# Kernel optimization log

Hardware: AMD Instinct MI355X
Metric: run time of the kernel (lower is better)

Reference implementation:

```python
import jax, jax.numpy as jnp
import numpy as np

B, N, T, C = 16, 12, 128, 128  # batch, num_classes (nodes), temporal, channels


def _bn(x, gamma, beta, eps=1e-5):
    # BatchNorm2d in training mode: stats over (batch, t, c), channel axis 1, biased var
    mean = jnp.mean(x, axis=(0, 2, 3), keepdims=True)
    var = jnp.var(x, axis=(0, 2, 3), keepdims=True)
    xn = (x - mean) * jax.lax.rsqrt(var + eps)
    return xn * gamma[None, :, None, None] + beta[None, :, None, None]


def setup_inputs() -> dict:
    key = jax.random.key(0)
    ks = jax.random.split(key, 3)
    scale = np.float32(np.sqrt(2.0 / C))
    inp = {
        'x': jax.random.normal(ks[0], (B, N, T, C), dtype=jnp.float32),
        'edge': jax.random.normal(ks[1], (B, N * N, T, C), dtype=jnp.float32),
    }
    wk = jax.random.split(ks[2], 10)
    for name, k in zip(['A1', 'B1', 'E1', 'U1', 'V1', 'A2', 'B2', 'E2', 'U2', 'V2'], wk):
        inp[name] = jax.random.normal(k, (C, C), dtype=jnp.float32) * scale
    for name, dim in [('g_e1', N * N), ('b_e1', N * N), ('g_v1', N), ('b_v1', N),
                      ('g_e2', N * N), ('b_e2', N * N), ('g_v2', N), ('b_v2', N)]:
        inp[name] = jnp.ones((dim,), jnp.float32) if name[0] == 'g' else jnp.zeros((dim,), jnp.float32)
    return inp


def _forward(x, edge, A1, B1, E1, U1, V1, A2, B2, E2, U2, V2,
             g_e1, b_e1, g_v1, b_v1, g_e2, b_e2, g_v2, b_v2):
    # create_e_matrix: edge index e = i*N + j; 'end' selects node i, 'start' selects node j.
    # Dense incidence einsums become pure gathers; the transpose einsum is a
    # scatter-add over j, i.e. a reshape + sum.
    i_idx = jnp.repeat(jnp.arange(N), N)  # end-node of each edge
    j_idx = jnp.tile(jnp.arange(N), N)    # start-node of each edge
    b, _, t, c = x.shape

    def layer(x, edge, A, Bw, E, U, V, ge, be, gv, bv, mask_node):
        res = x
        edge_upd = (x @ A.T)[:, i_idx] + (x @ Bw.T)[:, j_idx] + edge @ E.T
        edge_upd = _bn(edge_upd, ge, be)
        edge_upd = jnp.where(jnp.isnan(edge_upd), 0.0, edge_upd)
        edge = edge + jax.nn.relu(edge_upd)
        e = jax.nn.sigmoid(edge)
        e = jax.nn.softmax(e.reshape(b, N, N, t, c), axis=2).reshape(b, N * N, t, c)
        Ujx = (x @ V.T)[:, j_idx]
        agg = (e * Ujx).reshape(b, N, N, t, c).sum(axis=2) / N  # scatter to end nodes
        xn = _bn(x @ U.T + agg, gv, bv)
        if mask_node:  # original only NaN-masks node BN in layer 1
            xn = jnp.where(jnp.isnan(xn), 0.0, xn)
        return jax.nn.relu(res + xn), edge

    x, edge = layer(x, edge, A1, B1, E1, U1, V1, g_e1, b_e1, g_v1, b_v1, True)
    x, edge = layer(x, edge, A2, B2, E2, U2, V2, g_e2, b_e2, g_v2, b_v2, False)
    return x, edge


def reference(x, edge, A1, B1, E1, U1, V1, A2, B2, E2, U2, V2,
              g_e1, b_e1, g_v1, b_v1, g_e2, b_e2, g_v2, b_v2):
    return _forward(x, edge, A1, B1, E1, U1, V1, A2, B2, E2, U2, V2,
                    g_e1, b_e1, g_v1, b_v1, g_e2, b_e2, g_v2, b_v2)
```

## Files before the change

### kernel.cpp

```cpp
#include <hip/hip_runtime.h>
#include <hip/hip_bf16.h>

#define BB 16
#define NN 12
#define NE 144
#define TT 128
#define CC 128

typedef __attribute__((ext_vector_type(8))) short v8s;
typedef __attribute__((ext_vector_type(4))) short v4s;
typedef __attribute__((ext_vector_type(4))) float v4f;

__device__ __forceinline__ short f2bf(float f) {
    unsigned u = __float_as_uint(f);
    u += 0x7fffu + ((u >> 16) & 1u);
    return (short)(u >> 16);
}
__device__ __forceinline__ float bf2f(unsigned short u) {
    return __uint_as_float(((unsigned)u) << 16);
}
__device__ __forceinline__ v4s f4_to_bf4(float4 a) {
    v4s r; r[0] = f2bf(a.x); r[1] = f2bf(a.y); r[2] = f2bf(a.z); r[3] = f2bf(a.w); return r;
}
__device__ __forceinline__ float4 bf4_to_f4(v4s a) {
    float4 r;
    r.x = bf2f((unsigned short)a[0]); r.y = bf2f((unsigned short)a[1]);
    r.z = bf2f((unsigned short)a[2]); r.w = bf2f((unsigned short)a[3]);
    return r;
}
__device__ __forceinline__ size_t eslot(int b, int e, int t) {
    return ((((size_t)b * NE + e) * TT + t) * CC) * 2;
}

__global__ __launch_bounds__(256) void kW(
    const float* A1, const float* B1, const float* E1, const float* U1, const float* V1,
    const float* A2, const float* B2, const float* E2, const float* U2, const float* V2,
    unsigned short* wb)
{
    int idx = blockIdx.x * 256 + threadIdx.x;
    int w = idx >> 14, r = idx & 16383;
    const float* s;
    switch (w) {
        case 0: s = A1; break; case 1: s = B1; break; case 2: s = E1; break;
        case 3: s = U1; break; case 4: s = V1; break; case 5: s = A2; break;
        case 6: s = B2; break; case 7: s = E2; break; case 8: s = U2; break;
        default: s = V2; break;
    }
    wb[idx] = (unsigned short)f2bf(s[r]);
}

__global__ __launch_bounds__(256) void kP(
    const float* __restrict__ x, const unsigned short* __restrict__ wb,
    int sA, int sB, int sV, int sU,
    unsigned short* __restrict__ oA, unsigned short* __restrict__ oB,
    unsigned short* __restrict__ oV, unsigned short* __restrict__ oU)
{
    __shared__ unsigned short xt[64][136];
    int tid = threadIdx.x;
    int m0 = blockIdx.x * 64;
    #pragma unroll
    for (int it = 0; it < 8; ++it) {
        int f = it * 256 + tid;
        int row = f >> 5, c4 = f & 31;
        float4 v = *reinterpret_cast<const float4*>(x + (size_t)m0 * 128 + (size_t)f * 4);
        *reinterpret_cast<v4s*>(&xt[row][c4 * 4]) = f4_to_bf4(v);
    }
    __syncthreads();
    int lane = tid & 63, wid = tid >> 6;
    int l15 = lane & 15, l4 = lane >> 4;

    const unsigned short* Ws[4] = { wb + (size_t)sA * 16384, wb + (size_t)sB * 16384,
                                    wb + (size_t)sV * 16384, wb + (size_t)sU * 16384 };
    unsigned short* Os[4] = { oA, oB, oV, oU };

    #pragma unroll
    for (int w = 0; w < 4; ++w) {
        const unsigned short* W = Ws[w];
        unsigned short* out = Os[w];
        v8s bfr[2][4];
        #pragma unroll
        for (int nt2 = 0; nt2 < 2; ++nt2) {
            int col = (wid * 2 + nt2) * 16 + l15;
            #pragma unroll
            for (int kk = 0; kk < 4; ++kk)
                bfr[nt2][kk] = *reinterpret_cast<const v8s*>(W + col * 128 + kk * 32 + l4 * 8);
        }
        v4f acc[4][2] = {};
        #pragma unroll
        for (int kk = 0; kk < 4; ++kk) {
            #pragma unroll
            for (int mt = 0; mt < 4; ++mt) {
                v8s a = *reinterpret_cast<const v8s*>(&xt[mt * 16 + l15][kk * 32 + l4 * 8]);
                acc[mt][0] = __builtin_amdgcn_mfma_f32_16x16x32_bf16(a, bfr[0][kk], acc[mt][0], 0, 0, 0);
                acc[mt][1] = __builtin_amdgcn_mfma_f32_16x16x32_bf16(a, bfr[1][kk], acc[mt][1], 0, 0, 0);
            }
        }
        #pragma unroll
        for (int mt = 0; mt < 4; ++mt) {
            #pragma unroll
            for (int nt2 = 0; nt2 < 2; ++nt2) {
                int col = (wid * 2 + nt2) * 16 + l15;
                #pragma unroll
                for (int reg = 0; reg < 4; ++reg) {
                    int rowg = m0 + mt * 16 + l4 * 4 + reg;
                    out[(size_t)rowg * 128 + col] = (unsigned short)f2bf(acc[mt][nt2][reg]);
                }
            }
        }
    }
}

template<bool IN_F32>
__global__ __launch_bounds__(256) void kA(
    const float* __restrict__ ef32, const unsigned short* ebf,
    unsigned short* ebout,
    const unsigned short* __restrict__ xA, const unsigned short* __restrict__ xB,
    const unsigned short* __restrict__ Ebf, float* __restrict__ epart)
{
    __shared__ unsigned short ebt[48][136];
    __shared__ float4 xab4[16][33];
    __shared__ float srow[48], qrow[48];
    int tid = threadIdx.x;
    int bid = blockIdx.x;
    int third = bid % 3; int bt = bid / 3;
    int b = bt >> 7, t = bt & 127;
    if (tid < 48) { srow[tid] = 0.f; qrow[tid] = 0.f; }

    if constexpr (IN_F32) {
        const float* eb = ef32 + (((size_t)(b * NE + third * 48) * TT) + t) * CC;
        #pragma unroll
        for (int it = 0; it < 6; ++it) {
            int f = it * 256 + tid;
            int row = f >> 5, c4 = f & 31;
            float4 v = *reinterpret_cast<const float4*>(eb + (size_t)row * (TT * CC) + c4 * 4);
            *reinterpret_cast<v4s*>(&ebt[row][c4 * 4]) = f4_to_bf4(v);
        }
    } else {
        #pragma unroll
        for (int it = 0; it < 3; ++it) {
            int f = it * 256 + tid;
            int row = f >> 4, c8 = f & 15;
            *reinterpret_cast<v8s*>(&ebt[row][c8 * 8]) =
                *reinterpret_cast<const v8s*>(ebf + eslot(b, third * 48 + row, t) + c8 * 8);
        }
    }
    #pragma unroll
    for (int it = 0; it < 2; ++it) {
        int f = it * 256 + tid;
        int row = f >> 5, c4 = f & 31;
        const unsigned short* src = (row < 4)
            ? (xA + (((size_t)(b * NN + third * 4 + row) * TT) + t) * CC)
            : (xB + (((size_t)(b * NN + (row - 4)) * TT) + t) * CC);
        v4s v = *reinterpret_cast<const v4s*>(src + c4 * 4);
        xab4[row][c4] = bf4_to_f4(v);
    }
    __syncthreads();
    if constexpr (IN_F32) {
        #pragma unroll
        for (int it = 0; it < 3; ++it) {
            int f = it * 256 + tid;
            int row = f >> 4, c8 = f & 15;
            *reinterpret_cast<v8s*>(ebout + eslot(b, third * 48 + row, t) + c8 * 8) =
                *reinterpret_cast<const v8s*>(&ebt[row][c8 * 8]);
        }
    }
    int lane = tid & 63, wid = tid >> 6;
    int l15 = lane & 15, l4 = lane >> 4;
    v8s bfr[2][4];
    #pragma unroll
    for (int nt2 = 0; nt2 < 2; ++nt2) {
        int col = (wid * 2 + nt2) * 16 + l15;
        #pragma unroll
        for (int kk = 0; kk < 4; ++kk)
            bfr[nt2][kk] = *reinterpret_cast<const v8s*>(Ebf + col * 128 + kk * 32 + l4 * 8);
    }
    v4f acc[3][2] = {};
    #pragma unroll
    for (int kk = 0; kk < 4; ++kk) {
        #pragma unroll
        for (int mt = 0; mt < 3; ++mt) {
            v8s a = *reinterpret_cast<const v8s*>(&ebt[mt * 16 + l15][kk * 32 + l4 * 8]);
            acc[mt][0] = __builtin_amdgcn_mfma_f32_16x16x32_bf16(a, bfr[0][kk], acc[mt][0], 0, 0, 0);
            acc[mt][1] = __builtin_amdgcn_mfma_f32_16x16x32_bf16(a, bfr[1][kk], acc[mt][1], 0, 0, 0);
        }
    }
    const float* xabf = reinterpret_cast<const float*>(xab4);
    #pragma unroll
    for (int mt = 0; mt < 3; ++mt) {
        #pragma unroll
        for (int reg = 0; reg < 4; ++reg) {
            int r = mt * 16 + l4 * 4 + reg;
            int il = r / 12, jl = r - il * 12;
            float s = 0.f, q = 0.f;
            #pragma unroll
            for (int nt2 = 0; nt2 < 2; ++nt2) {
                int col = (wid * 2 + nt2) * 16 + l15;
                float v = acc[mt][nt2][reg] + xabf[il * 132 + col] + xabf[(4 + jl) * 132 + col];
                s += v; q += v * v;
            }
            #pragma unroll
            for (int off = 1; off < 16; off <<= 1) { s += __shfl_xor(s, off); q += __shfl_xor(q, off); }
            if (l15 == 0) { atomicAdd(&srow[r], s); atomicAdd(&qrow[r], q); }
        }
    }
    __syncthreads();
    if (tid < 48) {
        epart[(size_t)bid * 96 + tid * 2 + 0] = srow[tid];
        epart[(size_t)bid * 96 + tid * 2 + 1] = qrow[tid];
    }
}

__global__ __launch_bounds__(256) void kRede(
    const float* __restrict__ epart, const float* __restrict__ g,
    const float* __restrict__ be, float* __restrict__ estats)
{
    int e = blockIdx.x;
    int third = e / 48, le = e % 48;
    float s = 0.f, q = 0.f;
    for (int bt = threadIdx.x; bt < 2048; bt += 256) {
        const float* p = epart + ((size_t)(bt * 3 + third) * 96 + le * 2);
        s += p[0]; q += p[1];
    }
    __shared__ float ss[4], qq[4];
    #pragma unroll
    for (int off = 32; off >= 1; off >>= 1) { s += __shfl_down(s, off); q += __shfl_down(q, off); }
    int wid = threadIdx.x >> 6;
    if ((threadIdx.x & 63) == 0) { ss[wid] = s; qq[wid] = q; }
    __syncthreads();
    if (threadIdx.x == 0) {
        s = ss[0] + ss[1] + ss[2] + ss[3];
        q = qq[0] + qq[1] + qq[2] + qq[3];
        const float M = 262144.f;
        float mean = s / M;
        float var = q / M - mean * mean;
        float sc = g[e] * rsqrtf(var + 1e-5f);
        estats[e * 2] = sc;
        estats[e * 2 + 1] = be[e] - mean * sc;
    }
}

template<bool OUT_F32>
__global__ __launch_bounds__(256) void kC(
    const unsigned short* ebuf,
    unsigned short* ebout_bf,
    float* edge_out_f32,
    const unsigned short* __restrict__ xA, const unsigned short* __restrict__ xB,
    const unsigned short* __restrict__ xV, const unsigned short* __restrict__ xU,
    const unsigned short* __restrict__ Ebf, const float* __restrict__ estats,
    unsigned short* __restrict__ yout, float* __restrict__ npart)
{
    __shared__ unsigned short ebt[48][136];
    __shared__ float4 xab4[28][33];
    __shared__ float scs[48], shs[48];
    __shared__ float ns[4], nq[4];
    int tid = threadIdx.x;
    int bid = blockIdx.x;
    int third = bid % 3; int bt = bid / 3;
    int b = bt >> 7, t = bt & 127;
    if (tid < 48) { scs[tid] = estats[(third * 48 + tid) * 2]; shs[tid] = estats[(third * 48 + tid) * 2 + 1]; }
    if (tid < 4) { ns[tid] = 0.f; nq[tid] = 0.f; }
    #pragma unroll
    for (int it = 0; it < 3; ++it) {
        int f = it * 256 + tid;
        int row = f >> 4, c8 = f & 15;
        *reinterpret_cast<v8s*>(&ebt[row][c8 * 8]) =
            *reinterpret_cast<const v8s*>(ebuf + eslot(b, third * 48 + row, t) + c8 * 8);
    }
    #pragma unroll
    for (int it = 0; it < 4; ++it) {
        int f = it * 256 + tid;
        if (f < 896) {
            int row = f >> 5, c4 = f & 31;
            const unsigned short* src;
            if (row < 4)       src = xA + (((size_t)(b * NN + third * 4 + row) * TT) + t) * CC;
            else if (row < 16) src = xB + (((size_t)(b * NN + (row - 4)) * TT) + t) * CC;
            else               src = xV + (((size_t)(b * NN + (row - 16)) * TT) + t) * CC;
            v4s v = *reinterpret_cast<const v4s*>(src + c4 * 4);
            xab4[row][c4] = bf4_to_f4(v);
        }
    }
    __syncthreads();
    int lane = tid & 63, wid = tid >> 6;
    int l15 = lane & 15, l4 = lane >> 4;
    v8s bfr[2][4];
    #pragma unroll
    for (int nt2 = 0; nt2 < 2; ++nt2) {
        int col = (wid * 2 + nt2) * 16 + l15;
        #pragma unroll
        for (int kk = 0; kk < 4; ++kk)
            bfr[nt2][kk] = *reinterpret_cast<const v8s*>(Ebf + col * 128 + kk * 32 + l4 * 8);
    }
    v4f acc[3][2] = {};
    #pragma unroll
    for (int kk = 0; kk < 4; ++kk) {
        #pragma unroll
        for (int mt = 0; mt < 3; ++mt) {
            v8s a = *reinterpret_cast<const v8s*>(&ebt[mt * 16 + l15][kk * 32 + l4 * 8]);
            acc[mt][0] = __builtin_amdgcn_mfma_f32_16x16x32_bf16(a, bfr[0][kk], acc[mt][0], 0, 0, 0);
            acc[mt][1] = __builtin_amdgcn_mfma_f32_16x16x32_bf16(a, bfr[1][kk], acc[mt][1], 0, 0, 0);
        }
    }
    __syncthreads();
    const float* xabf = reinterpret_cast<const float*>(xab4);
    #pragma unroll
    for (int mt = 0; mt < 3; ++mt) {
        #pragma unroll
        for (int reg = 0; reg < 4; ++reg) {
            int r = mt * 16 + l4 * 4 + reg;
            int il = r / 12, jl = r - il * 12;
            int eg = third * 48 + r;
            float scv = scs[r], shv = shs[r];
            #pragma unroll
            for (int nt2 = 0; nt2 < 2; ++nt2) {
                int col = (wid * 2 + nt2) * 16 + l15;
                float v = acc[mt][nt2][reg] + xabf[il * 132 + col] + xabf[(4 + jl) * 132 + col];
                float bn = scv * v + shv;
                float en = bf2f(ebt[r][col]) + fmaxf(bn, 0.f);
                ebt[r][col] = (unsigned short)f2bf(en);
                if constexpr (OUT_F32)
                    edge_out_f32[((size_t)(b * NE + eg) * TT + t) * CC + col] = en;
            }
        }
    }
    __syncthreads();
    if constexpr (!OUT_F32) {
        #pragma unroll
        for (int it = 0; it < 3; ++it) {
            int f = it * 256 + tid;
            int row = f >> 4, c8 = f & 15;
            *reinterpret_cast<v8s*>(ebout_bf + eslot(b, third * 48 + row, t) + c8 * 8) =
                *reinterpret_cast<const v8s*>(&ebt[row][c8 * 8]);
        }
    }
    #pragma unroll
    for (int ph = 0; ph < 2; ++ph) {
        int unit = tid + ph * 256;
        int il = unit >> 7, c = unit & 127;
        float den = 0.f, ag = 0.f;
        #pragma unroll
        for (int j = 0; j < 12; ++j) {
            float sv = bf2f(ebt[il * 12 + j][c]);
            float sg = 1.f / (1.f + __expf(-sv));
            float ev = __expf(sg);
            den += ev;
            ag += ev * xabf[(16 + j) * 132 + c];
        }
        float agg = ag / (den * 12.f);
        int i = third * 4 + il;
        size_t xa = (((size_t)(b * NN + i) * TT) + t) * CC + c;
        float yv = bf2f(xU[xa]) + agg;
        unsigned short us = (unsigned short)f2bf(yv);
        yout[xa] = us;
        float yr = bf2f(us);
        float s1 = yr, s2 = yr * yr;
        #pragma unroll
        for (int off = 1; off < 64; off <<= 1) { s1 += __shfl_xor(s1, off); s2 += __shfl_xor(s2, off); }
        if (lane == 0) { atomicAdd(&ns[il], s1); atomicAdd(&nq[il], s2); }
    }
    __syncthreads();
    if (tid < 4) {
        npart[(size_t)bid * 8 + tid * 2 + 0] = ns[tid];
        npart[(size_t)bid * 8 + tid * 2 + 1] = nq[tid];
    }
}

__global__ __launch_bounds__(256) void kRedn(
    const float* __restrict__ npart, const float* __restrict__ g,
    const float* __restrict__ be, float* __restrict__ nstats)
{
    int n = blockIdx.x;
    int third = n >> 2, il = n & 3;
    float s = 0.f, q = 0.f;
    for (int bt = threadIdx.x; bt < 2048; bt += 256) {
        const float* p = npart + ((size_t)(bt * 3 + third) * 8 + il * 2);
        s += p[0]; q += p[1];
    }
    __shared__ float ss[4], qq[4];
    #pragma unroll
    for (int off = 32; off >= 1; off >>= 1) { s += __shfl_down(s, off); q += __shfl_down(q, off); }
    int wid = threadIdx.x >> 6;
    if ((threadIdx.x & 63) == 0) { ss[wid] = s; qq[wid] = q; }
    __syncthreads();
    if (threadIdx.x == 0) {
        s = ss[0] + ss[1] + ss[2] + ss[3];
        q = qq[0] + qq[1] + qq[2] + qq[3];
        const float M = 262144.f;
        float mean = s / M;
        float var = q / M - mean * mean;
        float sc = g[n] * rsqrtf(var + 1e-5f);
        nstats[n * 2] = sc;
        nstats[n * 2 + 1] = be[n] - mean * sc;
    }
}

__global__ __launch_bounds__(256) void kE(
    const float* xres, const unsigned short* __restrict__ yin,
    const float* __restrict__ nstats, float* xout)
{
    int idx4 = blockIdx.x * 256 + threadIdx.x;
    size_t base = (size_t)idx4 * 4;
    int n = (int)((base >> 14) % 12);
    float scv = nstats[n * 2], shv = nstats[n * 2 + 1];
    float4 xv = *reinterpret_cast<const float4*>(xres + base);
    float4 yv = bf4_to_f4(*reinterpret_cast<const v4s*>(yin + base));
    float4 o;
    o.x = fmaxf(xv.x + scv * yv.x + shv, 0.f);
    o.y = fmaxf(xv.y + scv * yv.y + shv, 0.f);
    o.z = fmaxf(xv.z + scv * yv.z + shv, 0.f);
    o.w = fmaxf(xv.w + scv * yv.w + shv, 0.f);
    *reinterpret_cast<float4*>(xout + base) = o;
}

extern "C" void kernel_launch(void* const* d_in, const int* in_sizes, int n_in,
                              void* d_out, int out_size, void* d_ws, size_t ws_size,
                              hipStream_t stream)
{
    const float* x0 = (const float*)d_in[0];
    const float* e0 = (const float*)d_in[1];
    const float* W[10];
    for (int i = 0; i < 10; ++i) W[i] = (const float*)d_in[2 + i];
    const float* ge1 = (const float*)d_in[12];
    const float* be1 = (const float*)d_in[13];
    const float* gv1 = (const float*)d_in[14];
    const float* bv1 = (const float*)d_in[15];
    const float* ge2 = (const float*)d_in[16];
    const float* be2 = (const float*)d_in[17];
    const float* gv2 = (const float*)d_in[18];
    const float* bv2 = (const float*)d_in[19];

    const size_t SZX = (size_t)BB * NN * TT * CC;
    float* out_x = (float*)d_out;
    float* out_e = out_x + SZX;
    unsigned short* ebuf = (unsigned short*)out_e;

    unsigned short* ws16 = (unsigned short*)d_ws;
    unsigned short* xA = ws16;
    unsigned short* xB = ws16 + SZX;
    unsigned short* xV = ws16 + 2 * SZX;
    unsigned short* xU = ws16 + 3 * SZX;
    unsigned short* yb = ws16 + 4 * SZX;
    float* fpart  = (float*)(ws16 + 5 * SZX);
    float* epart  = fpart;
    float* estats = epart + 589824;
    float* npart  = estats + 288;
    float* nstats = npart + 49152;
    unsigned short* wb = (unsigned short*)(nstats + 24);

    float* x1 = out_x;

    kW<<<640, 256, 0, stream>>>(W[0], W[1], W[2], W[3], W[4], W[5], W[6], W[7], W[8], W[9], wb);

    kP<<<384, 256, 0, stream>>>(x0, wb, 0, 1, 4, 3, xA, xB, xV, xU);
    kA<true><<<6144, 256, 0, stream>>>(e0, nullptr, ebuf, xA, xB, wb + 2 * 16384, epart);
    kRede<<<144, 256, 0, stream>>>(epart, ge1, be1, estats);
    kC<false><<<6144, 256, 0, stream>>>(ebuf, ebuf, nullptr, xA, xB, xV, xU,
                                        wb + 2 * 16384, estats, yb, npart);
    kRedn<<<12, 256, 0, stream>>>(npart, gv1, bv1, nstats);
    kE<<<3072, 256, 0, stream>>>(x0, yb, nstats, x1);

    kP<<<384, 256, 0, stream>>>(x1, wb, 5, 6, 9, 8, xA, xB, xV, xU);
    kA<false><<<6144, 256, 0, stream>>>(nullptr, ebuf, nullptr, xA, xB, wb + 7 * 16384, epart);
    kRede<<<144, 256, 0, stream>>>(epart, ge2, be2, estats);
    kC<true><<<6144, 256, 0, stream>>>(ebuf, nullptr, out_e, xA, xB, xV, xU,
                                       wb + 7 * 16384, estats, yb, npart);
    kRedn<<<12, 256, 0, stream>>>(npart, gv2, bv2, nstats);
    kE<<<3072, 256, 0, stream>>>(x1, yb, nstats, out_x);
}
```

Measured before the change: 310.1 us.

## Store pre-BN edge update in kA instead of recomputing GEMM in kC

```diff
diff --git a/kernel.cpp b/kernel.cpp
--- a/kernel.cpp
+++ b/kernel.cpp
@@ -22,14 +22,8 @@
 __device__ __forceinline__ v4s f4_to_bf4(float4 a) {
     v4s r; r[0] = f2bf(a.x); r[1] = f2bf(a.y); r[2] = f2bf(a.z); r[3] = f2bf(a.w); return r;
 }
-__device__ __forceinline__ float4 bf4_to_f4(v4s a) {
-    float4 r;
-    r.x = bf2f((unsigned short)a[0]); r.y = bf2f((unsigned short)a[1]);
-    r.z = bf2f((unsigned short)a[2]); r.w = bf2f((unsigned short)a[3]);
-    return r;
-}
-__device__ __forceinline__ size_t eslot(int b, int e, int t) {
-    return ((((size_t)b * NE + e) * TT + t) * CC) * 2;
+__device__ __forceinline__ size_t ebfslot(int b, int e, int t) {
+    return (((size_t)(b * NE + e) * TT) + t) * CC;
 }
 
 __global__ __launch_bounds__(256) void kW(
@@ -112,13 +106,14 @@
 
 template<bool IN_F32>
 __global__ __launch_bounds__(256) void kA(
-    const float* __restrict__ ef32, const unsigned short* ebf,
-    unsigned short* ebout,
+    const float* __restrict__ ef32, const unsigned short* __restrict__ ebf_in,
+    unsigned short* __restrict__ ebf_out,
+    unsigned short* __restrict__ updg,
     const unsigned short* __restrict__ xA, const unsigned short* __restrict__ xB,
     const unsigned short* __restrict__ Ebf, float* __restrict__ epart)
 {
     __shared__ unsigned short ebt[48][136];
-    __shared__ float4 xab4[16][33];
+    __shared__ unsigned short xab[16][136];
     __shared__ float srow[48], qrow[48];
     int tid = threadIdx.x;
     int bid = blockIdx.x;
@@ -127,7 +122,7 @@
     if (tid < 48) { srow[tid] = 0.f; qrow[tid] = 0.f; }
 
     if constexpr (IN_F32) {
-        const float* eb = ef32 + (((size_t)(b * NE + third * 48) * TT) + t) * CC;
+        const float* eb = ef32 + ebfslot(b, third * 48, t);
         #pragma unroll
         for (int it = 0; it < 6; ++it) {
             int f = it * 256 + tid;
@@ -141,18 +136,15 @@
             int f = it * 256 + tid;
             int row = f >> 4, c8 = f & 15;
             *reinterpret_cast<v8s*>(&ebt[row][c8 * 8]) =
-                *reinterpret_cast<const v8s*>(ebf + eslot(b, third * 48 + row, t) + c8 * 8);
-        }
-    }
-    #pragma unroll
-    for (int it = 0; it < 2; ++it) {
-        int f = it * 256 + tid;
-        int row = f >> 5, c4 = f & 31;
+                *reinterpret_cast<const v8s*>(ebf_in + ebfslot(b, third * 48 + row, t) + c8 * 8);
+        }
+    }
+    {
+        int row = tid >> 4, c8 = tid & 15;
         const unsigned short* src = (row < 4)
             ? (xA + (((size_t)(b * NN + third * 4 + row) * TT) + t) * CC)
             : (xB + (((size_t)(b * NN + (row - 4)) * TT) + t) * CC);
-        v4s v = *reinterpret_cast<const v4s*>(src + c4 * 4);
-        xab4[row][c4] = bf4_to_f4(v);
+        *reinterpret_cast<v8s*>(&xab[row][c8 * 8]) = *reinterpret_cast<const v8s*>(src + c8 * 8);
     }
     __syncthreads();
     if constexpr (IN_F32) {
@@ -160,7 +152,7 @@
         for (int it = 0; it < 3; ++it) {
             int f = it * 256 + tid;
             int row = f >> 4, c8 = f & 15;
-            *reinterpret_cast<v8s*>(ebout + eslot(b, third * 48 + row, t) + c8 * 8) =
+            *reinterpret_cast<v8s*>(ebf_out + ebfslot(b, third * 48 + row, t) + c8 * 8) =
                 *reinterpret_cast<const v8s*>(&ebt[row][c8 * 8]);
         }
     }
@@ -184,7 +176,7 @@
             acc[mt][1] = __builtin_amdgcn_mfma_f32_16x16x32_bf16(a, bfr[1][kk], acc[mt][1], 0, 0, 0);
         }
     }
-    const float* xabf = reinterpret_cast<const float*>(xab4);
+    __syncthreads();
     #pragma unroll
     for (int mt = 0; mt < 3; ++mt) {
         #pragma unroll
@@ -195,8 +187,9 @@
             #pragma unroll
             for (int nt2 = 0; nt2 < 2; ++nt2) {
                 int col = (wid * 2 + nt2) * 16 + l15;
-                float v = acc[mt][nt2][reg] + xabf[il * 132 + col] + xabf[(4 + jl) * 132 + col];
+                float v = acc[mt][nt2][reg] + bf2f(xab[il][col]) + bf2f(xab[4 + jl][col]);
                 s += v; q += v * v;
+                ebt[r][col] = (unsigned short)f2bf(v);
             }
             #pragma unroll
             for (int off = 1; off < 16; off <<= 1) { s += __shfl_xor(s, off); q += __shfl_xor(q, off); }
@@ -204,6 +197,13 @@
         }
     }
     __syncthreads();
+    #pragma unroll
+    for (int it = 0; it < 3; ++it) {
+        int f = it * 256 + tid;
+        int row = f >> 4, c8 = f & 15;
+        *reinterpret_cast<v8s*>(updg + (size_t)bid * 6144 + (size_t)f * 8) =
+            *reinterpret_cast<const v8s*>(&ebt[row][c8 * 8]);
+    }
     if (tid < 48) {
         epart[(size_t)bid * 96 + tid * 2 + 0] = srow[tid];
         epart[(size_t)bid * 96 + tid * 2 + 1] = qrow[tid];
@@ -241,16 +241,16 @@
 
 template<bool OUT_F32>
 __global__ __launch_bounds__(256) void kC(
-    const unsigned short* ebuf,
-    unsigned short* ebout_bf,
-    float* edge_out_f32,
-    const unsigned short* __restrict__ xA, const unsigned short* __restrict__ xB,
+    const unsigned short* __restrict__ ebf,
+    unsigned short* __restrict__ ebf_out,
+    float* __restrict__ eout,
+    const unsigned short* __restrict__ updg,
     const unsigned short* __restrict__ xV, const unsigned short* __restrict__ xU,
-    const unsigned short* __restrict__ Ebf, const float* __restrict__ estats,
+    const float* __restrict__ estats,
     unsigned short* __restrict__ yout, float* __restrict__ npart)
 {
-    __shared__ unsigned short ebt[48][136];
-    __shared__ float4 xab4[28][33];
+    __shared__ unsigned short se[48][136];
+    __shared__ unsigned short xv[12][136];
     __shared__ float scs[48], shs[48];
     __shared__ float ns[4], nq[4];
     int tid = threadIdx.x;
@@ -259,79 +259,39 @@
     int b = bt >> 7, t = bt & 127;
     if (tid < 48) { scs[tid] = estats[(third * 48 + tid) * 2]; shs[tid] = estats[(third * 48 + tid) * 2 + 1]; }
     if (tid < 4) { ns[tid] = 0.f; nq[tid] = 0.f; }
+    if (tid < 192) {
+        int row = tid >> 4, c8 = tid & 15;
+        *reinterpret_cast<v8s*>(&xv[row][c8 * 8]) =
+            *reinterpret_cast<const v8s*>(xV + (((size_t)(b * NN + row) * TT) + t) * CC + c8 * 8);
+    }
+    __syncthreads();
     #pragma unroll
     for (int it = 0; it < 3; ++it) {
         int f = it * 256 + tid;
         int row = f >> 4, c8 = f & 15;
-        *reinterpret_cast<v8s*>(&ebt[row][c8 * 8]) =
-            *reinterpret_cast<const v8s*>(ebuf + eslot(b, third * 48 + row, t) + c8 * 8);
-    }
-    #pragma unroll
-    for (int it = 0; it < 4; ++it) {
-        int f = it * 256 + tid;
-        if (f < 896) {
-            int row = f >> 5, c4 = f & 31;
-            const unsigned short* src;
-            if (row < 4)       src = xA + (((size_t)(b * NN + third * 4 + row) * TT) + t) * CC;
-            else if (row < 16) src = xB + (((size_t)(b * NN + (row - 4)) * TT) + t) * CC;
-            else               src = xV + (((size_t)(b * NN + (row - 16)) * TT) + t) * CC;
-            v4s v = *reinterpret_cast<const v4s*>(src + c4 * 4);
-            xab4[row][c4] = bf4_to_f4(v);
-        }
-    }
-    __syncthreads();
-    int lane = tid & 63, wid = tid >> 6;
-    int l15 = lane & 15, l4 = lane >> 4;
-    v8s bfr[2][4];
-    #pragma unroll
-    for (int nt2 = 0; nt2 < 2; ++nt2) {
-        int col = (wid * 2 + nt2) * 16 + l15;
-        #pragma unroll
-        for (int kk = 0; kk < 4; ++kk)
-            bfr[nt2][kk] = *reinterpret_cast<const v8s*>(Ebf + col * 128 + kk * 32 + l4 * 8);
-    }
-    v4f acc[3][2] = {};
-    #pragma unroll
-    for (int kk = 0; kk < 4; ++kk) {
-        #pragma unroll
-        for (int mt = 0; mt < 3; ++mt) {
-            v8s a = *reinterpret_cast<const v8s*>(&ebt[mt * 16 + l15][kk * 32 + l4 * 8]);
-            acc[mt][0] = __builtin_amdgcn_mfma_f32_16x16x32_bf16(a, bfr[0][kk], acc[mt][0], 0, 0, 0);
-            acc[mt][1] = __builtin_amdgcn_mfma_f32_16x16x32_bf16(a, bfr[1][kk], acc[mt][1], 0, 0, 0);
-        }
-    }
-    __syncthreads();
-    const float* xabf = reinterpret_cast<const float*>(xab4);
-    #pragma unroll
-    for (int mt = 0; mt < 3; ++mt) {
-        #pragma unroll
-        for (int reg = 0; reg < 4; ++reg) {
-            int r = mt * 16 + l4 * 4 + reg;
-            int il = r / 12, jl = r - il * 12;
-            int eg = third * 48 + r;
-            float scv = scs[r], shv = shs[r];
-            #pragma unroll
-            for (int nt2 = 0; nt2 < 2; ++nt2) {
-                int col = (wid * 2 + nt2) * 16 + l15;
-                float v = acc[mt][nt2][reg] + xabf[il * 132 + col] + xabf[(4 + jl) * 132 + col];
-                float bn = scv * v + shv;
-                float en = bf2f(ebt[r][col]) + fmaxf(bn, 0.f);
-                ebt[r][col] = (unsigned short)f2bf(en);
-                if constexpr (OUT_F32)
-                    edge_out_f32[((size_t)(b * NE + eg) * TT + t) * CC + col] = en;
-            }
-        }
-    }
-    __syncthreads();
-    if constexpr (!OUT_F32) {
-        #pragma unroll
-        for (int it = 0; it < 3; ++it) {
-            int f = it * 256 + tid;
-            int row = f >> 4, c8 = f & 15;
-            *reinterpret_cast<v8s*>(ebout_bf + eslot(b, third * 48 + row, t) + c8 * 8) =
-                *reinterpret_cast<const v8s*>(&ebt[row][c8 * 8]);
-        }
-    }
+        int eg = third * 48 + row;
+        v8s uv = *reinterpret_cast<const v8s*>(updg + (size_t)bid * 6144 + (size_t)f * 8);
+        size_t slot = ebfslot(b, eg, t) + c8 * 8;
+        v8s evv = *reinterpret_cast<const v8s*>(ebf + slot);
+        float sc = scs[row], sh = shs[row];
+        float en[8];
+        v8s nv;
+        #pragma unroll
+        for (int k = 0; k < 8; ++k) {
+            en[k] = bf2f((unsigned short)evv[k]) + fmaxf(sc * bf2f((unsigned short)uv[k]) + sh, 0.f);
+            nv[k] = f2bf(en[k]);
+        }
+        *reinterpret_cast<v8s*>(&se[row][c8 * 8]) = nv;
+        if constexpr (OUT_F32) {
+            size_t off = (((size_t)(b * NE + eg) * TT) + t) * CC + c8 * 8;
+            *reinterpret_cast<float4*>(eout + off)     = make_float4(en[0], en[1], en[2], en[3]);
+            *reinterpret_cast<float4*>(eout + off + 4) = make_float4(en[4], en[5], en[6], en[7]);
+        } else {
+            *reinterpret_cast<v8s*>(ebf_out + slot) = nv;
+        }
+    }
+    __syncthreads();
+    int lane = tid & 63;
     #pragma unroll
     for (int ph = 0; ph < 2; ++ph) {
         int unit = tid + ph * 256;
@@ -339,11 +299,11 @@
         float den = 0.f, ag = 0.f;
         #pragma unroll
         for (int j = 0; j < 12; ++j) {
-            float sv = bf2f(ebt[il * 12 + j][c]);
+            float sv = bf2f(se[il * 12 + j][c]);
             float sg = 1.f / (1.f + __expf(-sv));
             float ev = __expf(sg);
             den += ev;
-            ag += ev * xabf[(16 + j) * 132 + c];
+            ag += ev * bf2f(xv[j][c]);
         }
         float agg = ag / (den * 12.f);
         int i = third * 4 + il;
@@ -402,12 +362,12 @@
     int n = (int)((base >> 14) % 12);
     float scv = nstats[n * 2], shv = nstats[n * 2 + 1];
     float4 xv = *reinterpret_cast<const float4*>(xres + base);
-    float4 yv = bf4_to_f4(*reinterpret_cast<const v4s*>(yin + base));
+    v4s yv4 = *reinterpret_cast<const v4s*>(yin + base);
     float4 o;
-    o.x = fmaxf(xv.x + scv * yv.x + shv, 0.f);
-    o.y = fmaxf(xv.y + scv * yv.y + shv, 0.f);
-    o.z = fmaxf(xv.z + scv * yv.z + shv, 0.f);
-    o.w = fmaxf(xv.w + scv * yv.w + shv, 0.f);
+    o.x = fmaxf(xv.x + scv * bf2f((unsigned short)yv4[0]) + shv, 0.f);
+    o.y = fmaxf(xv.y + scv * bf2f((unsigned short)yv4[1]) + shv, 0.f);
+    o.z = fmaxf(xv.z + scv * bf2f((unsigned short)yv4[2]) + shv, 0.f);
+    o.w = fmaxf(xv.w + scv * bf2f((unsigned short)yv4[3]) + shv, 0.f);
     *reinterpret_cast<float4*>(xout + base) = o;
 }
 
@@ -429,9 +389,9 @@
     const float* bv2 = (const float*)d_in[19];
 
     const size_t SZX = (size_t)BB * NN * TT * CC;
+    const size_t SZE = (size_t)BB * NE * TT * CC;
     float* out_x = (float*)d_out;
     float* out_e = out_x + SZX;
-    unsigned short* ebuf = (unsigned short*)out_e;
 
     unsigned short* ws16 = (unsigned short*)d_ws;
     unsigned short* xA = ws16;
@@ -439,7 +399,9 @@
     unsigned short* xV = ws16 + 2 * SZX;
     unsigned short* xU = ws16 + 3 * SZX;
     unsigned short* yb = ws16 + 4 * SZX;
-    float* fpart  = (float*)(ws16 + 5 * SZX);
+    unsigned short* ebf = ws16 + 5 * SZX;
+    unsigned short* upd = ebf + SZE;
+    float* fpart  = (float*)(upd + SZE);
     float* epart  = fpart;
     float* estats = epart + 589824;
     float* npart  = estats + 288;
@@ -451,18 +413,16 @@
     kW<<<640, 256, 0, stream>>>(W[0], W[1], W[2], W[3], W[4], W[5], W[6], W[7], W[8], W[9], wb);
 
     kP<<<384, 256, 0, stream>>>(x0, wb, 0, 1, 4, 3, xA, xB, xV, xU);
-    kA<true><<<6144, 256, 0, stream>>>(e0, nullptr, ebuf, xA, xB, wb + 2 * 16384, epart);
+    kA<true><<<6144, 256, 0, stream>>>(e0, nullptr, ebf, upd, xA, xB, wb + 2 * 16384, epart);
     kRede<<<144, 256, 0, stream>>>(epart, ge1, be1, estats);
-    kC<false><<<6144, 256, 0, stream>>>(ebuf, ebuf, nullptr, xA, xB, xV, xU,
-                                        wb + 2 * 16384, estats, yb, npart);
+    kC<false><<<6144, 256, 0, stream>>>(ebf, ebf, nullptr, upd, xV, xU, estats, yb, npart);
     kRedn<<<12, 256, 0, stream>>>(npart, gv1, bv1, nstats);
     kE<<<3072, 256, 0, stream>>>(x0, yb, nstats, x1);
 
     kP<<<384, 256, 0, stream>>>(x1, wb, 5, 6, 9, 8, xA, xB, xV, xU);
-    kA<false><<<6144, 256, 0, stream>>>(nullptr, ebuf, nullptr, xA, xB, wb + 7 * 16384, epart);
+    kA<false><<<6144, 256, 0, stream>>>(nullptr, ebf, nullptr, upd, xA, xB, wb + 7 * 16384, epart);
     kRede<<<144, 256, 0, stream>>>(epart, ge2, be2, estats);
-    kC<true><<<6144, 256, 0, stream>>>(ebuf, nullptr, out_e, xA, xB, xV, xU,
-                                       wb + 7 * 16384, estats, yb, npart);
+    kC<true><<<6144, 256, 0, stream>>>(ebf, nullptr, out_e, upd, xV, xU, estats, yb, npart);
     kRedn<<<12, 256, 0, stream>>>(npart, gv2, bv2, nstats);
     kE<<<3072, 256, 0, stream>>>(x1, yb, nstats, out_x);
 }
```

Measured after the change: 309.8 us. Within noise of the previous version (-0.1%).
